# Optimization experiments

Hardware: AMD Instinct MI355X
Metric: run time of the kernel (lower is better)

Reference implementation:

```python
import jax, jax.numpy as jnp
import numpy as np

B, T, I, H, O = 64, 512, 512, 1024, 512


def setup_inputs() -> dict:
    key = jax.random.key(0)
    ks = jax.random.split(key, 11)
    s_gate = 1.0 / np.sqrt(I + H)
    s_fc = 1.0 / np.sqrt(H)
    return {
        "x": jax.random.normal(ks[0], (B, T, I), dtype=jnp.float32),
        "W_f": jax.random.uniform(ks[1], (H, I + H), jnp.float32, -s_gate, s_gate),
        "b_f": jax.random.uniform(ks[2], (H,), jnp.float32, -s_gate, s_gate),
        "W_i": jax.random.uniform(ks[3], (H, I + H), jnp.float32, -s_gate, s_gate),
        "b_i": jax.random.uniform(ks[4], (H,), jnp.float32, -s_gate, s_gate),
        "W_c": jax.random.uniform(ks[5], (H, I + H), jnp.float32, -s_gate, s_gate),
        "b_c": jax.random.uniform(ks[6], (H,), jnp.float32, -s_gate, s_gate),
        "W_o": jax.random.uniform(ks[7], (H, I + H), jnp.float32, -s_gate, s_gate),
        "b_o": jax.random.uniform(ks[8], (H,), jnp.float32, -s_gate, s_gate),
        "W_fc": jax.random.uniform(ks[9], (O, H), jnp.float32, -s_fc, s_fc),
        "b_fc": jax.random.uniform(ks[10], (O,), jnp.float32, -s_fc, s_fc),
    }


def reference(x, W_f, b_f, W_i, b_i, W_c, b_c, W_o, b_o, W_fc, b_fc):
    batch = x.shape[0]
    hidden = W_f.shape[0]
    # Concatenate the 4 gate weights into one GEMM per step (same math).
    W_all = jnp.concatenate([W_f, W_i, W_c, W_o], axis=0)   # [4H, I+H]
    b_all = jnp.concatenate([b_f, b_i, b_c, b_o], axis=0)   # [4H]

    def step(carry, x_t):
        h, c = carry
        combined = jnp.concatenate([x_t, h], axis=1)         # [B, I+H]
        gates = combined @ W_all.T + b_all                   # [B, 4H]
        f_t = jax.nn.sigmoid(gates[:, :hidden])
        i_t = jax.nn.sigmoid(gates[:, hidden:2 * hidden])
        c_tilde = jnp.tanh(gates[:, 2 * hidden:3 * hidden])
        o_t = jax.nn.sigmoid(gates[:, 3 * hidden:])
        c_new = f_t * c + i_t * c_tilde
        h_new = o_t * jnp.tanh(c_new)
        y = h_new @ W_fc.T + b_fc                            # [B, O]
        return (h_new, c_new), y

    h0 = jnp.zeros((batch, hidden), x.dtype)
    c0 = jnp.zeros((batch, hidden), x.dtype)
    (h, c), ys = jax.lax.scan(step, (h0, c0), jnp.swapaxes(x, 0, 1))
    return jnp.swapaxes(ys, 0, 1), (h, c)
```

## Files before the change

### kernel.cpp

```cpp
#include <hip/hip_runtime.h>
#include <stdint.h>

#define BB 64
#define TT 512
#define II 512
#define HH 1024
#define OO 512
#define NBLK 256
#define NTHR 256
#define NB 16
#define US 16

#define WS_HBUF  1280
#define WS_ASLAB 66816
#define WS_YSLAB 3212544
#define BTO (BB*TT*OO)
#define BH  (BB*HH)

#define L_HB_U4 1024
#define L_YP_F  12288
#define L_BYTES ((12288 + 1280) * 4)

typedef __fp16 v8hf __attribute__((ext_vector_type(8)));
typedef float f32x4 __attribute__((ext_vector_type(4)));
typedef _Float16 h2 __attribute__((ext_vector_type(2)));

static __device__ __forceinline__ v8hf bc8(uint4 v) { return __builtin_bit_cast(v8hf, v); }
static __device__ __forceinline__ uint32_t pk_u32(float a, float b) {
  return __builtin_bit_cast(uint32_t, __builtin_amdgcn_cvt_pkrtz(a, b));
}

__device__ __forceinline__ float sigm(float v) { return 1.0f / (1.0f + __expf(-v)); }
__device__ __forceinline__ float tanh_c(float v) {
  v = fminf(fmaxf(v, -20.0f), 20.0f);
  float e = __expf(-2.0f * v);
  return (1.0f - e) / (1.0f + e);
}

__device__ __forceinline__ uint2 cohere_ld8(const void* p) {
  unsigned long long q = __hip_atomic_load((const unsigned long long*)p,
                                           __ATOMIC_RELAXED, __HIP_MEMORY_SCOPE_AGENT);
  return __builtin_bit_cast(uint2, q);
}
__device__ __forceinline__ void cohere_st8(void* p, uint32_t lo, uint32_t hi) {
  uint2 v = make_uint2(lo, hi);
  __hip_atomic_store((unsigned long long*)p, __builtin_bit_cast(unsigned long long, v),
                     __ATOMIC_RELAXED, __HIP_MEMORY_SCOPE_AGENT);
}

__global__ void __launch_bounds__(256) prep(
    const float* __restrict__ Wf, const float* __restrict__ Wi,
    const float* __restrict__ Wc, const float* __restrict__ Wo,
    const float* __restrict__ Wfc, float* __restrict__ ws)
{
  const int NA = 64 * 4 * 48 * 64;
  const int NY = 64 * 32 * 64;
  int idx = blockIdx.x * 256 + threadIdx.x;
  if (idx < NA) {
    int s = idx / (4 * 48 * 64);
    int rem = idx % (4 * 48 * 64);
    int mt = rem / (48 * 64);
    int rem2 = rem % (48 * 64);
    int ks = rem2 >> 6, ln = rem2 & 63;
    int r = ln & 15, kq = ln >> 4;
    int unit = s * 16 + mt * 4 + (r >> 2), gate = r & 3;
    const float* W = (gate == 0) ? Wf : (gate == 1) ? Wi : (gate == 2) ? Wc : Wo;
    const float* src = W + (size_t)unit * 1536 + ks * 32 + kq * 8;
    uint32_t p[4];
    #pragma unroll
    for (int j = 0; j < 4; ++j) {
      h2 t; t.x = (_Float16)src[2*j]; t.y = (_Float16)src[2*j+1];
      p[j] = __builtin_bit_cast(uint32_t, t);
    }
    ((uint4*)(ws + WS_ASLAB))[idx] = make_uint4(p[0], p[1], p[2], p[3]);
  } else if (idx < NA + NY) {
    int j2 = idx - NA;
    int s = j2 / (32 * 64);
    int rem = j2 % (32 * 64);
    int ks = rem >> 6, ln = rem & 63;
    int r = ln & 15, kq = ln >> 4;
    uint4 outv = make_uint4(0, 0, 0, 0);
    if (r < 8) {
      const float* src = Wfc + (size_t)(s * 8 + r) * 1024 + ks * 32 + kq * 8;
      uint32_t p[4];
      #pragma unroll
      for (int j = 0; j < 4; ++j) {
        h2 t; t.x = (_Float16)src[2*j]; t.y = (_Float16)src[2*j+1];
        p[j] = __builtin_bit_cast(uint32_t, t);
      }
      outv = make_uint4(p[0], p[1], p[2], p[3]);
    }
    ((uint4*)(ws + WS_YSLAB))[j2] = outv;
  }
}

__global__ void __launch_bounds__(NTHR, 1)
lstm_kernel(const float* __restrict__ x,
            const float* __restrict__ bf, const float* __restrict__ bi,
            const float* __restrict__ bc, const float* __restrict__ bo,
            const float* __restrict__ bfc,
            float* __restrict__ out, float* __restrict__ ws)
{
  extern __shared__ float ldsf[];
  uint4* acts4 = (uint4*)ldsf;
  float* ypart = ldsf + L_YP_F;

  const int tid  = threadIdx.x;
  const int blk  = blockIdx.x;
  const int wave = tid >> 6;
  const int lane = tid & 63;
  const int g = blk >> 6, s = blk & 63;
  const int b0 = g * NB;
  const int u0 = s * US;

  uint32_t* ctrl  = (uint32_t*)ws;
  uint32_t* rootp = ctrl + g * 32;
  ushort* hb16 = (ushort*)(ws + WS_HBUF);

  const int bq = lane & 15, kq = lane >> 4;
  const int sb = tid >> 4, sj = tid & 15;

  v8hf Aw[48];
  v8hf Yw[8];
  {
    const uint4* wpA = (const uint4*)(ws + WS_ASLAB) + ((size_t)(s * 4 + wave) * 48) * 64 + lane;
    #pragma unroll
    for (int k = 0; k < 48; ++k) Aw[k] = bc8(wpA[k * 64]);
    const uint4* wpY = (const uint4*)(ws + WS_YSLAB) + ((size_t)(s * 32 + wave * 8)) * 64 + lane;
    #pragma unroll
    for (int k = 0; k < 8; ++k) Yw[k] = bc8(wpY[k * 64]);
  }
  const int unit = u0 + wave * 4 + kq;
  const float bsf = bf[unit], bsi = bi[unit], bsc = bc[unit], bso = bo[unit];
  const float ybias = (tid < 128) ? bfc[s * 8 + (tid >> 4)] : 0.0f;
  float cstate = 0.0f;
  f32x4 xacc[4];

  {
    const float* xs = x + ((size_t)(b0 + sb) * TT + 0) * II + sj * 32;
    #pragma unroll
    for (int v = 0; v < 4; ++v) {
      float4 u = ((const float4*)xs)[2*v], w = ((const float4*)xs)[2*v+1];
      acts4[sj * 64 + v * 16 + (sb ^ (sj & 7))] =
          make_uint4(pk_u32(u.x,u.y), pk_u32(u.z,u.w), pk_u32(w.x,w.y), pk_u32(w.z,w.w));
    }
    #pragma unroll
    for (int w = 0; w < 8; ++w) {
      int khb = sj * 2 + (w >> 2);
      acts4[L_HB_U4 + khb * 64 + (w & 3) * 16 + (sb ^ (khb & 7))] = make_uint4(0,0,0,0);
    }
  }
  __syncthreads();
  {
    #pragma unroll
    for (int j = 0; j < 4; ++j) xacc[j] = (f32x4){0.f, 0.f, 0.f, 0.f};
    #pragma unroll
    for (int ks = 0; ks < 16; ++ks) {
      uint4 bv = acts4[ks * 64 + kq * 16 + (bq ^ (ks & 7))];
      xacc[ks & 3] = __builtin_amdgcn_mfma_f32_16x16x32_f16(Aw[ks], bc8(bv), xacc[ks & 3], 0, 0, 0);
    }
  }

  for (int it = 0; it <= TT; ++it) {
    float4 xr[8];
    const bool xok = (it + 1 < TT);
    if (xok) {
      const float* xs = x + ((size_t)(b0 + sb) * TT + (it + 1)) * II + sj * 32;
      #pragma unroll
      for (int v = 0; v < 8; ++v) xr[v] = ((const float4*)xs)[v];
    }

    if (it < TT) {
      f32x4 ac[4];
      #pragma unroll
      for (int j = 0; j < 4; ++j) ac[j] = xacc[j];
      #pragma unroll
      for (int ksh = 0; ksh < 32; ++ksh) {
        uint4 bv = acts4[L_HB_U4 + ksh * 64 + kq * 16 + (bq ^ (ksh & 7))];
        ac[ksh & 3] = __builtin_amdgcn_mfma_f32_16x16x32_f16(Aw[16 + ksh], bc8(bv), ac[ksh & 3], 0, 0, 0);
      }
      f32x4 t = (ac[0] + ac[1]) + (ac[2] + ac[3]);

      float gf = sigm(t[0] + bsf);
      float gi = sigm(t[1] + bsi);
      float gc = tanh_c(t[2] + bsc);
      float go = sigm(t[3] + bso);
      cstate = gf * cstate + gi * gc;
      float hv = go * tanh_c(cstate);

      uint32_t hu = (uint32_t)__builtin_bit_cast(unsigned short, (_Float16)hv);
      uint32_t pA  = hu | ((uint32_t)__shfl_down((int)hu, 16) << 16);
      uint32_t hiw = (uint32_t)__shfl_down((int)pA, 32);
      if (kq == 0) {
        ushort* hp = hb16 + (size_t)((it + 1) & 1) * BH
                   + (size_t)(b0 + bq) * HH + (u0 + wave * 4);
        cohere_st8(hp, pA, hiw);
      }
      if (it == TT - 1) {
        out[(size_t)BTO + (size_t)(b0 + bq) * HH + unit] = hv;
        out[(size_t)BTO + BH + (size_t)(b0 + bq) * HH + unit] = cstate;
      }

      asm volatile("s_waitcnt vmcnt(0)" ::: "memory");
      __syncthreads();
      if (tid == 0)
        (void)__hip_atomic_fetch_add(rootp, 1u, __ATOMIC_RELAXED, __HIP_MEMORY_SCOPE_AGENT);
    }


    if (it > 0) {
      f32x4 yc = (f32x4){0.f, 0.f, 0.f, 0.f};
      #pragma unroll
      for (int k = 0; k < 8; ++k) {
        int ksh = wave * 8 + k;
        uint4 bv = acts4[L_HB_U4 + ksh * 64 + kq * 16 + (bq ^ (ksh & 7))];
        yc = __builtin_amdgcn_mfma_f32_16x16x32_f16(Yw[k], bc8(bv), yc, 0, 0, 0);
      }
      float* yp = ypart + (wave * 64 + lane) * 5;
      yp[0] = yc[0]; yp[1] = yc[1]; yp[2] = yc[2]; yp[3] = yc[3];
    }

    if (xok) {
      #pragma unroll
      for (int v = 0; v < 4; ++v)
        acts4[sj * 64 + v * 16 + (sb ^ (sj & 7))] =
            make_uint4(pk_u32(xr[2*v].x, xr[2*v].y), pk_u32(xr[2*v].z, xr[2*v].w),
                       pk_u32(xr[2*v+1].x, xr[2*v+1].y), pk_u32(xr[2*v+1].z, xr[2*v+1].w));
    }
    __syncthreads();

    if (it > 0 && tid < 128) {
      int fb = tid & 15, rr = tid >> 4;
      int l = (rr >> 2) * 16 + fb;
      float yv = ybias;
      #pragma unroll
      for (int w = 0; w < 4; ++w) yv += ypart[(w * 64 + l) * 5 + (rr & 3)];
      out[(size_t)(b0 + fb) * (TT * OO) + (size_t)(it - 1) * OO + s * 8 + rr] = yv;
    }

    if (xok) {
      #pragma unroll
      for (int j = 0; j < 4; ++j) xacc[j] = (f32x4){0.f, 0.f, 0.f, 0.f};
      #pragma unroll
      for (int ks = 0; ks < 16; ++ks) {
        uint4 bv = acts4[ks * 64 + kq * 16 + (bq ^ (ks & 7))];
        xacc[ks & 3] = __builtin_amdgcn_mfma_f32_16x16x32_f16(Aw[ks], bc8(bv), xacc[ks & 3], 0, 0, 0);
      }
    }

    if (it < TT) {
      {
        const uint32_t tgt = 64u * (uint32_t)(it + 1);
        while (__hip_atomic_load(rootp, __ATOMIC_RELAXED, __HIP_MEMORY_SCOPE_AGENT) < tgt)
          __builtin_amdgcn_s_sleep(1);
      }

      {
        const ushort* hs = hb16 + (size_t)((it + 1) & 1) * BH
                         + (size_t)(b0 + sb) * HH + sj * 64;
        uint2 q[16];
        #pragma unroll
        for (int m = 0; m < 16; ++m) q[m] = cohere_ld8(hs + m * 4);
        #pragma unroll
        for (int w = 0; w < 8; ++w) {
          int khb = sj * 2 + (w >> 2);
          acts4[L_HB_U4 + khb * 64 + (w & 3) * 16 + (sb ^ (khb & 7))] =
              make_uint4(q[2*w].x, q[2*w].y, q[2*w+1].x, q[2*w+1].y);
        }
      }
      __syncthreads();
    }
  }
}

extern "C" void kernel_launch(void* const* d_in, const int* in_sizes, int n_in,
                              void* d_out, int out_size, void* d_ws, size_t ws_size,
                              hipStream_t stream) {
  (void)in_sizes; (void)n_in; (void)out_size; (void)ws_size;
  const float* x   = (const float*)d_in[0];
  const float* Wf  = (const float*)d_in[1];
  const float* bf  = (const float*)d_in[2];
  const float* Wi  = (const float*)d_in[3];
  const float* bi  = (const float*)d_in[4];
  const float* Wc  = (const float*)d_in[5];
  const float* bc  = (const float*)d_in[6];
  const float* Wo  = (const float*)d_in[7];
  const float* bo  = (const float*)d_in[8];
  const float* Wfc = (const float*)d_in[9];
  const float* bfc = (const float*)d_in[10];
  float* out = (float*)d_out;
  float* ws  = (float*)d_ws;

  (void)hipMemsetAsync(d_ws, 0, (size_t)WS_HBUF * sizeof(float), stream);

  const int nprep = 64 * 4 * 48 * 64 + 64 * 32 * 64;
  prep<<<dim3((nprep + 255) / 256), dim3(256), 0, stream>>>(Wf, Wi, Wc, Wo, Wfc, ws);

  lstm_kernel<<<dim3(NBLK), dim3(NTHR), L_BYTES, stream>>>(
      x, bf, bi, bc, bo, bfc, out, ws);
}
```

Measured before the change: 3.737 ms.

## Split block into gate waves and helper waves for x-projection and output FC

Doubles the block to 512 threads and specializes waves: four waves hold only the recurrent h-weights and compute gates, while four helper waves hold the x-weights and FC weights. The helper waves compute the next step's x-projection into LDS and the output projection, and all eight waves split the h-gather from global memory. The goal is to take x-projection and FC work off the critical recurrent path and to lower per-wave register pressure. In exchange it adds an extra barrier per step and an LDS round trip for the x contribution.

New measurement: 3.374 ms. 9.7% less time.

```diff
diff --git a/kernel.cpp b/kernel.cpp
--- a/kernel.cpp
+++ b/kernel.cpp
@@ -7,7 +7,7 @@
 #define HH 1024
 #define OO 512
 #define NBLK 256
-#define NTHR 256
+#define NTHR 512
 #define NB 16
 #define US 16
 
@@ -19,7 +19,8 @@
 
 #define L_HB_U4 1024
 #define L_YP_F  12288
-#define L_BYTES ((12288 + 1280) * 4)
+#define L_XP_F  (12288 + 1280)
+#define L_BYTES ((13568 + 1024) * 4)
 
 typedef __fp16 v8hf __attribute__((ext_vector_type(8)));
 typedef float f32x4 __attribute__((ext_vector_type(4)));
@@ -94,7 +95,7 @@
   }
 }
 
-__global__ void __launch_bounds__(NTHR, 1)
+__global__ void __launch_bounds__(NTHR, 2)
 lstm_kernel(const float* __restrict__ x,
             const float* __restrict__ bf, const float* __restrict__ bi,
             const float* __restrict__ bc, const float* __restrict__ bo,
@@ -104,11 +105,14 @@
   extern __shared__ float ldsf[];
   uint4* acts4 = (uint4*)ldsf;
   float* ypart = ldsf + L_YP_F;
+  float* xpart = ldsf + L_XP_F;
 
   const int tid  = threadIdx.x;
   const int blk  = blockIdx.x;
   const int wave = tid >> 6;
   const int lane = tid & 63;
+  const bool isGate = (wave < 4);
+  const int mt = wave & 3;
   const int g = blk >> 6, s = blk & 63;
   const int b0 = g * NB;
   const int u0 = s * US;
@@ -118,25 +122,37 @@
   ushort* hb16 = (ushort*)(ws + WS_HBUF);
 
   const int bq = lane & 15, kq = lane >> 4;
-  const int sb = tid >> 4, sj = tid & 15;
-
-  v8hf Aw[48];
+  const int tid2 = tid & 255;
+  const int sb = tid2 >> 4, sj = tid2 & 15;
+  const int gb = tid >> 5, gj = tid & 31;
+
+  v8hf Ah[32];
+  v8hf Ax[16];
   v8hf Yw[8];
-  {
-    const uint4* wpA = (const uint4*)(ws + WS_ASLAB) + ((size_t)(s * 4 + wave) * 48) * 64 + lane;
-    #pragma unroll
-    for (int k = 0; k < 48; ++k) Aw[k] = bc8(wpA[k * 64]);
-    const uint4* wpY = (const uint4*)(ws + WS_YSLAB) + ((size_t)(s * 32 + wave * 8)) * 64 + lane;
+  if (isGate) {
+    const uint4* wpA = (const uint4*)(ws + WS_ASLAB)
+                     + ((size_t)(s * 4 + mt) * 48 + 16) * 64 + lane;
+    #pragma unroll
+    for (int k = 0; k < 32; ++k) Ah[k] = bc8(wpA[k * 64]);
+  } else {
+    const uint4* wpA = (const uint4*)(ws + WS_ASLAB)
+                     + ((size_t)(s * 4 + mt) * 48) * 64 + lane;
+    #pragma unroll
+    for (int k = 0; k < 16; ++k) Ax[k] = bc8(wpA[k * 64]);
+    const uint4* wpY = (const uint4*)(ws + WS_YSLAB)
+                     + ((size_t)(s * 32 + mt * 8)) * 64 + lane;
     #pragma unroll
     for (int k = 0; k < 8; ++k) Yw[k] = bc8(wpY[k * 64]);
   }
-  const int unit = u0 + wave * 4 + kq;
-  const float bsf = bf[unit], bsi = bi[unit], bsc = bc[unit], bso = bo[unit];
+  const int unit = u0 + mt * 4 + kq;
+  const float bsf = isGate ? bf[unit] : 0.f;
+  const float bsi = isGate ? bi[unit] : 0.f;
+  const float bsc = isGate ? bc[unit] : 0.f;
+  const float bso = isGate ? bo[unit] : 0.f;
   const float ybias = (tid < 128) ? bfc[s * 8 + (tid >> 4)] : 0.0f;
   float cstate = 0.0f;
-  f32x4 xacc[4];
-
-  {
+
+  if (!isGate) {
     const float* xs = x + ((size_t)(b0 + sb) * TT + 0) * II + sj * 32;
     #pragma unroll
     for (int v = 0; v < 4; ++v) {
@@ -144,83 +160,97 @@
       acts4[sj * 64 + v * 16 + (sb ^ (sj & 7))] =
           make_uint4(pk_u32(u.x,u.y), pk_u32(u.z,u.w), pk_u32(w.x,w.y), pk_u32(w.z,w.w));
     }
-    #pragma unroll
-    for (int w = 0; w < 8; ++w) {
-      int khb = sj * 2 + (w >> 2);
-      acts4[L_HB_U4 + khb * 64 + (w & 3) * 16 + (sb ^ (khb & 7))] = make_uint4(0,0,0,0);
-    }
+  } else {
+    #pragma unroll
+    for (int j = 0; j < 8; ++j)
+      acts4[L_HB_U4 + tid2 * 8 + j] = make_uint4(0,0,0,0);
   }
   __syncthreads();
-  {
-    #pragma unroll
-    for (int j = 0; j < 4; ++j) xacc[j] = (f32x4){0.f, 0.f, 0.f, 0.f};
+  if (!isGate) {
+    f32x4 ac[4];
+    #pragma unroll
+    for (int j = 0; j < 4; ++j) ac[j] = (f32x4){0.f,0.f,0.f,0.f};
     #pragma unroll
     for (int ks = 0; ks < 16; ++ks) {
       uint4 bv = acts4[ks * 64 + kq * 16 + (bq ^ (ks & 7))];
-      xacc[ks & 3] = __builtin_amdgcn_mfma_f32_16x16x32_f16(Aw[ks], bc8(bv), xacc[ks & 3], 0, 0, 0);
-    }
-  }
+      ac[ks & 3] = __builtin_amdgcn_mfma_f32_16x16x32_f16(Ax[ks], bc8(bv), ac[ks & 3], 0, 0, 0);
+    }
+    f32x4 t = (ac[0] + ac[1]) + (ac[2] + ac[3]);
+    float* xp = xpart + (mt * 64 + lane) * 4;
+    xp[0] = t[0]; xp[1] = t[1]; xp[2] = t[2]; xp[3] = t[3];
+  }
+  __syncthreads();
 
   for (int it = 0; it <= TT; ++it) {
-    float4 xr[8];
     const bool xok = (it + 1 < TT);
-    if (xok) {
+
+    if (isGate) {
+      if (it < TT) {
+        const float* xp = xpart + (mt * 64 + lane) * 4;
+        f32x4 ac[4];
+        ac[0] = (f32x4){xp[0], xp[1], xp[2], xp[3]};
+        ac[1] = (f32x4){0.f,0.f,0.f,0.f};
+        ac[2] = (f32x4){0.f,0.f,0.f,0.f};
+        ac[3] = (f32x4){0.f,0.f,0.f,0.f};
+        #pragma unroll
+        for (int ksh = 0; ksh < 32; ++ksh) {
+          uint4 bv = acts4[L_HB_U4 + ksh * 64 + kq * 16 + (bq ^ (ksh & 7))];
+          ac[ksh & 3] = __builtin_amdgcn_mfma_f32_16x16x32_f16(Ah[ksh], bc8(bv), ac[ksh & 3], 0, 0, 0);
+        }
+        f32x4 t = (ac[0] + ac[1]) + (ac[2] + ac[3]);
+
+        float gf = sigm(t[0] + bsf);
+        float gi = sigm(t[1] + bsi);
+        float gc = tanh_c(t[2] + bsc);
+        float go = sigm(t[3] + bso);
+        cstate = gf * cstate + gi * gc;
+        float hv = go * tanh_c(cstate);
+
+        uint32_t hu = (uint32_t)__builtin_bit_cast(unsigned short, (_Float16)hv);
+        uint32_t pA  = hu | ((uint32_t)__shfl_down((int)hu, 16) << 16);
+        uint32_t hiw = (uint32_t)__shfl_down((int)pA, 32);
+        if (kq == 0) {
+          ushort* hp = hb16 + (size_t)((it + 1) & 1) * BH
+                     + (size_t)(b0 + bq) * HH + (u0 + mt * 4);
+          cohere_st8(hp, pA, hiw);
+        }
+        if (it == TT - 1) {
+          out[(size_t)BTO + (size_t)(b0 + bq) * HH + unit] = hv;
+          out[(size_t)BTO + BH + (size_t)(b0 + bq) * HH + unit] = cstate;
+        }
+        asm volatile("s_waitcnt vmcnt(0)" ::: "memory");
+      }
+    } else {
+      if (it > 0) {
+        f32x4 yc = (f32x4){0.f,0.f,0.f,0.f};
+        #pragma unroll
+        for (int k = 0; k < 8; ++k) {
+          int ksh = mt * 8 + k;
+          uint4 bv = acts4[L_HB_U4 + ksh * 64 + kq * 16 + (bq ^ (ksh & 7))];
+          yc = __builtin_amdgcn_mfma_f32_16x16x32_f16(Yw[k], bc8(bv), yc, 0, 0, 0);
+        }
+        float* yp = ypart + (mt * 64 + lane) * 5;
+        yp[0] = yc[0]; yp[1] = yc[1]; yp[2] = yc[2]; yp[3] = yc[3];
+      }
+    }
+    __syncthreads();
+
+    if (it < TT && tid == 0)
+      (void)__hip_atomic_fetch_add(rootp, 1u, __ATOMIC_RELAXED, __HIP_MEMORY_SCOPE_AGENT);
+
+    if (tid < 128 && it > 0) {
+      int fb = tid & 15, rr = tid >> 4;
+      int l = (rr >> 2) * 16 + fb;
+      float yv = ybias;
+      #pragma unroll
+      for (int w = 0; w < 4; ++w) yv += ypart[(w * 64 + l) * 5 + (rr & 3)];
+      out[(size_t)(b0 + fb) * (TT * OO) + (size_t)(it - 1) * OO + s * 8 + rr] = yv;
+    }
+    if (!isGate && xok) {
       const float* xs = x + ((size_t)(b0 + sb) * TT + (it + 1)) * II + sj * 32;
+      float4 xr[8];
       #pragma unroll
       for (int v = 0; v < 8; ++v) xr[v] = ((const float4*)xs)[v];
-    }
-
-    if (it < TT) {
-      f32x4 ac[4];
-      #pragma unroll
-      for (int j = 0; j < 4; ++j) ac[j] = xacc[j];
-      #pragma unroll
-      for (int ksh = 0; ksh < 32; ++ksh) {
-        uint4 bv = acts4[L_HB_U4 + ksh * 64 + kq * 16 + (bq ^ (ksh & 7))];
-        ac[ksh & 3] = __builtin_amdgcn_mfma_f32_16x16x32_f16(Aw[16 + ksh], bc8(bv), ac[ksh & 3], 0, 0, 0);
-      }
-      f32x4 t = (ac[0] + ac[1]) + (ac[2] + ac[3]);
-
-      float gf = sigm(t[0] + bsf);
-      float gi = sigm(t[1] + bsi);
-      float gc = tanh_c(t[2] + bsc);
-      float go = sigm(t[3] + bso);
-      cstate = gf * cstate + gi * gc;
-      float hv = go * tanh_c(cstate);
-
-      uint32_t hu = (uint32_t)__builtin_bit_cast(unsigned short, (_Float16)hv);
-      uint32_t pA  = hu | ((uint32_t)__shfl_down((int)hu, 16) << 16);
-      uint32_t hiw = (uint32_t)__shfl_down((int)pA, 32);
-      if (kq == 0) {
-        ushort* hp = hb16 + (size_t)((it + 1) & 1) * BH
-                   + (size_t)(b0 + bq) * HH + (u0 + wave * 4);
-        cohere_st8(hp, pA, hiw);
-      }
-      if (it == TT - 1) {
-        out[(size_t)BTO + (size_t)(b0 + bq) * HH + unit] = hv;
-        out[(size_t)BTO + BH + (size_t)(b0 + bq) * HH + unit] = cstate;
-      }
-
-      asm volatile("s_waitcnt vmcnt(0)" ::: "memory");
-      __syncthreads();
-      if (tid == 0)
-        (void)__hip_atomic_fetch_add(rootp, 1u, __ATOMIC_RELAXED, __HIP_MEMORY_SCOPE_AGENT);
-    }
-
-
-    if (it > 0) {
-      f32x4 yc = (f32x4){0.f, 0.f, 0.f, 0.f};
-      #pragma unroll
-      for (int k = 0; k < 8; ++k) {
-        int ksh = wave * 8 + k;
-        uint4 bv = acts4[L_HB_U4 + ksh * 64 + kq * 16 + (bq ^ (ksh & 7))];
-        yc = __builtin_amdgcn_mfma_f32_16x16x32_f16(Yw[k], bc8(bv), yc, 0, 0, 0);
-      }
-      float* yp = ypart + (wave * 64 + lane) * 5;
-      yp[0] = yc[0]; yp[1] = yc[1]; yp[2] = yc[2]; yp[3] = yc[3];
-    }
-
-    if (xok) {
       #pragma unroll
       for (int v = 0; v < 4; ++v)
         acts4[sj * 64 + v * 16 + (sb ^ (sj & 7))] =
@@ -229,44 +259,35 @@
     }
     __syncthreads();
 
-    if (it > 0 && tid < 128) {
-      int fb = tid & 15, rr = tid >> 4;
-      int l = (rr >> 2) * 16 + fb;
-      float yv = ybias;
-      #pragma unroll
-      for (int w = 0; w < 4; ++w) yv += ypart[(w * 64 + l) * 5 + (rr & 3)];
-      out[(size_t)(b0 + fb) * (TT * OO) + (size_t)(it - 1) * OO + s * 8 + rr] = yv;
-    }
-
-    if (xok) {
-      #pragma unroll
-      for (int j = 0; j < 4; ++j) xacc[j] = (f32x4){0.f, 0.f, 0.f, 0.f};
+    if (!isGate && xok) {
+      f32x4 ac[4];
+      #pragma unroll
+      for (int j = 0; j < 4; ++j) ac[j] = (f32x4){0.f,0.f,0.f,0.f};
       #pragma unroll
       for (int ks = 0; ks < 16; ++ks) {
         uint4 bv = acts4[ks * 64 + kq * 16 + (bq ^ (ks & 7))];
-        xacc[ks & 3] = __builtin_amdgcn_mfma_f32_16x16x32_f16(Aw[ks], bc8(bv), xacc[ks & 3], 0, 0, 0);
-      }
+        ac[ks & 3] = __builtin_amdgcn_mfma_f32_16x16x32_f16(Ax[ks], bc8(bv), ac[ks & 3], 0, 0, 0);
+      }
+      f32x4 t = (ac[0] + ac[1]) + (ac[2] + ac[3]);
+      float* xp = xpart + (mt * 64 + lane) * 4;
+      xp[0] = t[0]; xp[1] = t[1]; xp[2] = t[2]; xp[3] = t[3];
     }
 
     if (it < TT) {
-      {
-        const uint32_t tgt = 64u * (uint32_t)(it + 1);
-        while (__hip_atomic_load(rootp, __ATOMIC_RELAXED, __HIP_MEMORY_SCOPE_AGENT) < tgt)
-          __builtin_amdgcn_s_sleep(1);
-      }
+      const uint32_t tgt = 64u * (uint32_t)(it + 1);
+      while (__hip_atomic_load(rootp, __ATOMIC_RELAXED, __HIP_MEMORY_SCOPE_AGENT) < tgt)
+        __builtin_amdgcn_s_sleep(1);
 
       {
         const ushort* hs = hb16 + (size_t)((it + 1) & 1) * BH
-                         + (size_t)(b0 + sb) * HH + sj * 64;
-        uint2 q[16];
+                         + (size_t)(b0 + gb) * HH + gj * 32;
+        uint2 q[8];
         #pragma unroll
-        for (int m = 0; m < 16; ++m) q[m] = cohere_ld8(hs + m * 4);
+        for (int m = 0; m < 8; ++m) q[m] = cohere_ld8(hs + m * 4);
         #pragma unroll
-        for (int w = 0; w < 8; ++w) {
-          int khb = sj * 2 + (w >> 2);
-          acts4[L_HB_U4 + khb * 64 + (w & 3) * 16 + (sb ^ (khb & 7))] =
-              make_uint4(q[2*w].x, q[2*w].y, q[2*w+1].x, q[2*w+1].y);
-        }
+        for (int sub = 0; sub < 4; ++sub)
+          acts4[L_HB_U4 + gj * 64 + sub * 16 + (gb ^ (gj & 7))] =
+              make_uint4(q[2*sub].x, q[2*sub].y, q[2*sub+1].x, q[2*sub+1].y);
       }
       __syncthreads();
     }
```
